# Optimization experiments

Measured on AMD Instinct MI355X. Metric: run time of the kernel, lower is better.

The kernel has to match this reference:

```python
import jax, jax.numpy as jnp
import numpy as np

NUM_LAYERS = 4
OPTIONS = 32
SHAPE = (3, 32, 32)
D = int(np.prod(SHAPE))  # 3072
H = 256
B = 256


def setup_inputs() -> dict:
    key = jax.random.key(0)
    ks = jax.random.split(key, 4)
    inputs = jax.random.normal(ks[0], (B,) + SHAPE, dtype=jnp.float32)
    Wb = jax.random.normal(ks[1], (D, H), dtype=jnp.float32) * 0.02
    bb = jnp.zeros((H,), dtype=jnp.float32)
    Wo_stack = jax.random.normal(ks[2], (NUM_LAYERS, H, OPTIONS * D), dtype=jnp.float32) * 0.02
    bo_stack = jnp.zeros((NUM_LAYERS, OPTIONS * D), dtype=jnp.float32)
    bias_stack = jnp.zeros((NUM_LAYERS, OPTIONS, D), dtype=jnp.float32)
    return {"inputs": inputs, "Wb": Wb, "bb": bb, "Wo_stack": Wo_stack,
            "bo_stack": bo_stack, "bias_stack": bias_stack}


def reference(inputs, Wb, bb, Wo_stack, bo_stack, bias_stack):
    """Iterative residual vector quantization (VQ-DRAW encoder).

    Returns (encodings [B, num_layers] int32, reconstructions [B, *SHAPE]).
    """
    b = inputs.shape[0]
    x = inputs.reshape(b, D)                      # [B, D] flattened target
    cur = jnp.zeros_like(x)                       # current reconstruction
    encodings = []
    for i in range(NUM_LAYERS):
        base_out = jax.nn.relu(cur @ Wb + bb)                     # [B, H]
        layer_out = (base_out @ Wo_stack[i] + bo_stack[i])        # [B, O*D]
        layer_out = layer_out.reshape(b, OPTIONS, D) + bias_stack[i][None]
        new = cur[:, None, :] + layer_out                          # [B, O, D]
        # per-(example, option) MSE-sum loss, fused argmin over options
        losses = jnp.sum(jnp.square(new - x[:, None, :]), axis=-1)  # [B, O]
        idx = jnp.argmin(losses, axis=-1)                          # [B]
        encodings.append(idx)
        cur = jnp.take_along_axis(new, idx[:, None, None], axis=1)[:, 0]  # [B, D]
    return jnp.stack(encodings, axis=-1), cur.reshape(inputs.shape)
```

## Files before the change

### kernel.cpp

```cpp
#include <hip/hip_runtime.h>
#include <hip/hip_bf16.h>

#define B_ 256
#define D_ 3072
#define H_ 256
#define OPT_ 32
#define OD_ 98304
#define NL_ 4

typedef __attribute__((ext_vector_type(8))) short short8;
typedef __attribute__((ext_vector_type(4))) float f32x4;

__device__ __forceinline__ unsigned short f2bf(float f) {
    unsigned int u = __float_as_uint(f);
    unsigned int r = (u + 0x7FFFu + ((u >> 16) & 1u)) >> 16;
    return (unsigned short)r;
}

__global__ __launch_bounds__(256) void init_kernel(const float* __restrict__ x,
                                                   float* __restrict__ cur,
                                                   float* __restrict__ rx,
                                                   float* __restrict__ zpart) {
    int gid0 = blockIdx.x * 256 + threadIdx.x;
    for (int g = gid0; g < B_ * D_; g += 131072) {
        cur[g] = 0.f;
        rx[g] = -x[g];
    }
    for (int g = gid0; g < 16 * B_ * H_; g += 131072) zpart[g] = 0.f;
}

__global__ __launch_bounds__(256) void gemm1_kernel(const float* __restrict__ cur,
                                                    const float* __restrict__ Wb,
                                                    float* __restrict__ zpart) {
    int t = threadIdx.x;
    int ks = blockIdx.x >> 5;
    int bg = blockIdx.x & 31;
    const float* wp = Wb + (size_t)ks * 192 * H_ + t;
    const float* cp = cur + (size_t)(bg * 8) * D_ + ks * 192;
    float acc[8] = {0.f, 0.f, 0.f, 0.f, 0.f, 0.f, 0.f, 0.f};
#pragma unroll 4
    for (int dd = 0; dd < 192; ++dd) {
        float w = wp[(size_t)dd * H_];
#pragma unroll
        for (int g = 0; g < 8; ++g) acc[g] += cp[(size_t)g * D_ + dd] * w;
    }
#pragma unroll
    for (int g = 0; g < 8; ++g)
        zpart[ks * (B_ * H_) + (bg * 8 + g) * H_ + t] = acc[g];
}

__global__ __launch_bounds__(256) void e_kernel(const float* __restrict__ zpart,
                                                const float* __restrict__ bb,
                                                unsigned char* __restrict__ base_ready,
                                                float* __restrict__ basef) {
    int m = blockIdx.x, k = threadIdx.x;
    float z = bb[k];
#pragma unroll
    for (int ks = 0; ks < 16; ++ks) z += zpart[ks * (B_ * H_) + m * H_ + k];
    z = z > 0.f ? z : 0.f;
    *(unsigned short*)(base_ready + (k >> 5) * 20480 + m * 80 + (k & 31) * 2) = f2bf(z);
    basef[m * H_ + k] = z;
}

__global__ __launch_bounds__(512, 4) void g2_kernel(const unsigned char* __restrict__ base_ready,
                                                    const float* __restrict__ Wo,
                                                    const float* __restrict__ biasL,
                                                    const float* __restrict__ boL,
                                                    const float* __restrict__ rx,
                                                    float* __restrict__ partial) {
    __shared__ __align__(16) unsigned char ldsA[2][20480];
    __shared__ __align__(16) unsigned char ldsW[2][10240];

    int t = threadIdx.x;
    int lane = t & 63, wv = t >> 6;
    int bx = blockIdx.x;
    int ncol0 = bx * 128;
    int o = bx / 24;
    int dbase = (bx % 24) * 128;

    int wm = wv >> 1, wn = wv & 1;
    int lrow = lane & 15, lk = lane >> 4;
    int nW = t & 127, kq = t >> 7;

    f32x4 acc[4][4];
#pragma unroll
    for (int mi = 0; mi < 4; ++mi)
#pragma unroll
        for (int ni = 0; ni < 4; ++ni) acc[mi][ni] = 0.f;

    float wfX[8], wfY[8];

#define DMA_A(S, BUF) {                                                                  \
    const unsigned char* gA = base_ready + (S) * 20480;                                  \
    __builtin_amdgcn_global_load_lds(                                                    \
        (const __attribute__((address_space(1))) unsigned int*)(gA + t * 16),            \
        (__attribute__((address_space(3))) unsigned int*)(&ldsA[BUF][0] + wv * 1024),    \
        16, 0, 0);                                                                       \
    __builtin_amdgcn_global_load_lds(                                                    \
        (const __attribute__((address_space(1))) unsigned int*)(gA + 8192 + t * 16),     \
        (__attribute__((address_space(3))) unsigned int*)(&ldsA[BUF][0] + 8192 + wv * 1024), \
        16, 0, 0);                                                                       \
    if (wv < 4)                                                                          \
        __builtin_amdgcn_global_load_lds(                                                \
            (const __attribute__((address_space(1))) unsigned int*)(gA + 16384 + t * 16),\
            (__attribute__((address_space(3))) unsigned int*)(&ldsA[BUF][0] + 16384 + wv * 1024), \
            16, 0, 0); }

#define LOADW_(S, WF) {                                                                  \
    const float* gp0 = Wo + (size_t)((S) * 32 + kq * 4) * OD_ + ncol0 + nW;              \
    WF[0] = gp0[0]; WF[1] = gp0[OD_]; WF[2] = gp0[2 * OD_]; WF[3] = gp0[3 * OD_];        \
    const float* gp1 = gp0 + (size_t)16 * OD_;                                           \
    WF[4] = gp1[0]; WF[5] = gp1[OD_]; WF[6] = gp1[2 * OD_]; WF[7] = gp1[3 * OD_]; }

#define WRITEW_(BUF, WF) {                                                               \
    uint2 pk0, pk1;                                                                      \
    pk0.x = (unsigned)f2bf(WF[0]) | ((unsigned)f2bf(WF[1]) << 16);                       \
    pk0.y = (unsigned)f2bf(WF[2]) | ((unsigned)f2bf(WF[3]) << 16);                       \
    *(uint2*)(ldsW[BUF] + nW * 80 + kq * 8) = pk0;                                       \
    pk1.x = (unsigned)f2bf(WF[4]) | ((unsigned)f2bf(WF[5]) << 16);                       \
    pk1.y = (unsigned)f2bf(WF[6]) | ((unsigned)f2bf(WF[7]) << 16);                       \
    *(uint2*)(ldsW[BUF] + nW * 80 + 32 + kq * 8) = pk1; }

    DMA_A(0, 0);
    LOADW_(0, wfX);
    LOADW_(1, wfY);
    WRITEW_(0, wfX);
    asm volatile("s_waitcnt lgkmcnt(0)" ::: "memory");
    __builtin_amdgcn_s_barrier();

#pragma unroll 2
    for (int s = 0; s < 8; ++s) {
        int cur = s & 1;
        if (s < 7) DMA_A(s + 1, cur ^ 1);
        if (s < 6) {
            if ((s & 1) == 0) { LOADW_(s + 2, wfX); }
            else              { LOADW_(s + 2, wfY); }
        }
        short8 bfr[4];
#pragma unroll
        for (int ni = 0; ni < 4; ++ni) {
            int nn = wn * 64 + ni * 16 + lrow;
            bfr[ni] = *(const short8*)(ldsW[cur] + nn * 80 + lk * 16);
        }
#pragma unroll
        for (int mi = 0; mi < 4; ++mi) {
            int row = wm * 64 + mi * 16 + lrow;
            short8 af = *(const short8*)(ldsA[cur] + row * 80 + lk * 16);
#pragma unroll
            for (int ni = 0; ni < 4; ++ni)
                acc[mi][ni] = __builtin_amdgcn_mfma_f32_16x16x32_bf16(af, bfr[ni], acc[mi][ni], 0, 0, 0);
        }
        if (s < 7) {
            if ((s & 1) == 0) { WRITEW_(cur ^ 1, wfY); }
            else              { WRITEW_(cur ^ 1, wfX); }
            if (s < 6) asm volatile("s_waitcnt vmcnt(8) lgkmcnt(0)" ::: "memory");
            else       asm volatile("s_waitcnt vmcnt(0) lgkmcnt(0)" ::: "memory");
            __builtin_amdgcn_s_barrier();
        }
    }

#undef DMA_A
#undef LOADW_
#undef WRITEW_

    float q[4];
#pragma unroll
    for (int ni = 0; ni < 4; ++ni) {
        int dcol = dbase + wn * 64 + ni * 16 + lrow;
        q[ni] = biasL[o * D_ + dcol] + boL[o * D_ + dcol];
    }
    float ssum[4][4];
#pragma unroll
    for (int mi = 0; mi < 4; ++mi)
#pragma unroll
        for (int r = 0; r < 4; ++r) ssum[mi][r] = 0.f;

#pragma unroll
    for (int mi = 0; mi < 4; ++mi) {
#pragma unroll
        for (int ni = 0; ni < 4; ++ni) {
            int dcol = dbase + wn * 64 + ni * 16 + lrow;
#pragma unroll
            for (int r = 0; r < 4; ++r) {
                int rowm = wm * 64 + mi * 16 + lk * 4 + r;
                float tv = acc[mi][ni][r] + rx[rowm * D_ + dcol] + q[ni];
                ssum[mi][r] += tv * tv;
            }
        }
    }
#pragma unroll
    for (int mi = 0; mi < 4; ++mi)
#pragma unroll
        for (int r = 0; r < 4; ++r) {
            float v = ssum[mi][r];
            v += __shfl_xor(v, 1);
            v += __shfl_xor(v, 2);
            v += __shfl_xor(v, 4);
            v += __shfl_xor(v, 8);
            if (lrow == 0) {
                int rowm = wm * 64 + mi * 16 + lk * 4 + r;
                partial[(rowm * OPT_ + o) * 48 + (bx % 24) * 2 + wn] = v;
            }
        }
}

__global__ __launch_bounds__(256) void c_kernel(const float* __restrict__ partial,
                                                int* __restrict__ idxbuf,
                                                float* __restrict__ enc, int layer) {
    __shared__ float ls[32];
    int b = blockIdx.x, t = threadIdx.x;
    int oo = t >> 3, j8 = t & 7;
    const float* pp = partial + (b * OPT_ + oo) * 48;
    float v = 0.f;
#pragma unroll
    for (int j = 0; j < 6; ++j) v += pp[j8 + 8 * j];
    v += __shfl_xor(v, 1);
    v += __shfl_xor(v, 2);
    v += __shfl_xor(v, 4);
    if (j8 == 0) ls[oo] = v;
    __syncthreads();
    if (t < 32) {
        float mv = ls[t];
        int mi = t;
#pragma unroll
        for (int m = 16; m >= 1; m >>= 1) {
            float ov = __shfl_xor(mv, m);
            int oi = __shfl_xor(mi, m);
            if (ov < mv || (ov == mv && oi < mi)) { mv = ov; mi = oi; }
        }
        if (t == 0) {
            idxbuf[b] = mi;
            enc[b * NL_ + layer] = (float)mi;
        }
    }
}

__global__ __launch_bounds__(256) void d_kernel(const int* __restrict__ idxbuf,
                                                const float* __restrict__ basef,
                                                const float* __restrict__ Wo,
                                                const float* __restrict__ boL,
                                                const float* __restrict__ biasL,
                                                const float* __restrict__ x,
                                                float* __restrict__ cur,
                                                float* __restrict__ rx) {
    __shared__ int sidx[256];
    __shared__ int scnt[32];
    __shared__ int snch[32];
    __shared__ int chunk_b[8];
    __shared__ float basL[8][256];
    int t = threadIdx.x;
    int dt = blockIdx.y;

    sidx[t] = idxbuf[t];
    __syncthreads();
    if (t < 32) {
        int c = 0;
        for (int b = 0; b < 256; ++b) c += (sidx[b] == t);
        scnt[t] = c;
        snch[t] = (c + 7) >> 3;
    }
    __syncthreads();
    int myo = sidx[t];
    int myrank = 0;
    for (int b = 0; b < t; ++b) myrank += (sidx[b] == myo);

    for (int j = blockIdx.x; ; j += 32) {
        int o = -1, ch = 0, pre = 0;
        for (int oo = 0; oo < 32; ++oo) {
            int n = snch[oo];
            if (j < pre + n) { o = oo; ch = j - pre; break; }
            pre += n;
        }
        if (o < 0) break;
        int cnt = scnt[o];
        int c0 = ch * 8;
        int rem = cnt - c0;
        if (rem > 8) rem = 8;

        __syncthreads();
        if (myo == o && myrank >= c0 && myrank < c0 + 8) chunk_b[myrank - c0] = t;
        __syncthreads();

        int bidx[8];
#pragma unroll
        for (int g = 0; g < 8; ++g) bidx[g] = chunk_b[(g < rem) ? g : (rem - 1)];
#pragma unroll
        for (int g = 0; g < 8; ++g) basL[g][t] = basef[bidx[g] * H_ + t];
        __syncthreads();

        int d = dt * 256 + t;
        const float* wp = Wo + (size_t)o * D_ + d;
        size_t nn = (size_t)o * D_ + d;
        float bov = boL[nn];
        float biv = biasL[nn];

        float acc[8] = {0.f, 0.f, 0.f, 0.f, 0.f, 0.f, 0.f, 0.f};
        for (int k0 = 0; k0 < 256; k0 += 8) {
            float w[8];
#pragma unroll
            for (int u = 0; u < 8; ++u) w[u] = wp[(size_t)(k0 + u) * OD_];
#pragma unroll
            for (int h = 0; h < 2; ++h) {
                int kb = k0 + h * 4;
                f32x4 bv[8];
#pragma unroll
                for (int g = 0; g < 8; ++g) bv[g] = *(const f32x4*)&basL[g][kb];
#pragma unroll
                for (int u = 0; u < 4; ++u) {
                    float wu = w[h * 4 + u];
#pragma unroll
                    for (int g = 0; g < 8; ++g) acc[g] += bv[g][u] * wu;
                }
            }
        }
#pragma unroll
        for (int g = 0; g < 8; ++g) {
            if (g < rem) {
                int b = bidx[g];
                float outv = cur[b * D_ + d] + acc[g] + bov + biv;
                cur[b * D_ + d] = outv;
                rx[b * D_ + d] = outv - x[b * D_ + d];
            }
        }
    }
}

extern "C" void kernel_launch(void* const* d_in, const int* in_sizes, int n_in,
                              void* d_out, int out_size, void* d_ws, size_t ws_size,
                              hipStream_t stream) {
    const float* x    = (const float*)d_in[0];
    const float* Wb   = (const float*)d_in[1];
    const float* bb   = (const float*)d_in[2];
    const float* Wo   = (const float*)d_in[3];
    const float* bo   = (const float*)d_in[4];
    const float* bias = (const float*)d_in[5];

    float* out = (float*)d_out;
    float* enc = out;
    float* cur = out + 1024;

    float* ws = (float*)d_ws;
    float* zpart   = ws;
    float* partial = ws + 1048576;
    float* rx      = ws + 1441792;
    float* basef   = ws + 2228224;
    unsigned char* base_ready = (unsigned char*)(ws + 2293760);
    int* idxbuf    = (int*)(ws + 2334720);

    init_kernel<<<512, 256, 0, stream>>>(x, cur, rx, zpart);

    for (int i = 0; i < NL_; ++i) {
        const float* WoL   = Wo + (size_t)i * H_ * OD_;
        const float* boLp  = bo + (size_t)i * OD_;
        const float* biasL = bias + (size_t)i * OD_;
        if (i > 0) gemm1_kernel<<<512, 256, 0, stream>>>(cur, Wb, zpart);
        e_kernel<<<256, 256, 0, stream>>>(zpart, bb, base_ready, basef);
        g2_kernel<<<768, 512, 0, stream>>>(base_ready, WoL, biasL, boLp, rx, partial);
        c_kernel<<<256, 256, 0, stream>>>(partial, idxbuf, enc, i);
        d_kernel<<<dim3(32, 12), 256, 0, stream>>>(idxbuf, basef, WoL, boLp, biasL, x, cur, rx);
    }
}
```

Measured before the change: 390.7 us.

## Make g2 a persistent atomic-ticket tile loop and shrink small-kernel grids

The output-projection GEMM kernel now launches 512 persistent blocks that take further tiles from a per-layer atomic ticket counter instead of one block per tile. This is meant to reduce tail imbalance and launch overhead across the 768 tiles. gemm1 uses half as many K-splits (each twice as long), which halves the zpart partial buffer and the reduction work in e_kernel. e_kernel and c_kernel each handle four rows per block with smaller grids. The trade-off is less parallelism in gemm1 and an extra atomic plus block syncs per tile in g2.

```diff
diff --git a/kernel.cpp b/kernel.cpp
--- a/kernel.cpp
+++ b/kernel.cpp
@@ -20,13 +20,15 @@
 __global__ __launch_bounds__(256) void init_kernel(const float* __restrict__ x,
                                                    float* __restrict__ cur,
                                                    float* __restrict__ rx,
-                                                   float* __restrict__ zpart) {
+                                                   float* __restrict__ zpart,
+                                                   int* __restrict__ g2tk) {
     int gid0 = blockIdx.x * 256 + threadIdx.x;
-    for (int g = gid0; g < B_ * D_; g += 131072) {
+    for (int g = gid0; g < B_ * D_; g += 65536) {
         cur[g] = 0.f;
         rx[g] = -x[g];
     }
-    for (int g = gid0; g < 16 * B_ * H_; g += 131072) zpart[g] = 0.f;
+    for (int g = gid0; g < 8 * B_ * H_; g += 65536) zpart[g] = 0.f;
+    if (gid0 < NL_) g2tk[gid0] = 512;
 }
 
 __global__ __launch_bounds__(256) void gemm1_kernel(const float* __restrict__ cur,
@@ -35,11 +37,11 @@
     int t = threadIdx.x;
     int ks = blockIdx.x >> 5;
     int bg = blockIdx.x & 31;
-    const float* wp = Wb + (size_t)ks * 192 * H_ + t;
-    const float* cp = cur + (size_t)(bg * 8) * D_ + ks * 192;
+    const float* wp = Wb + (size_t)ks * 384 * H_ + t;
+    const float* cp = cur + (size_t)(bg * 8) * D_ + ks * 384;
     float acc[8] = {0.f, 0.f, 0.f, 0.f, 0.f, 0.f, 0.f, 0.f};
 #pragma unroll 4
-    for (int dd = 0; dd < 192; ++dd) {
+    for (int dd = 0; dd < 384; ++dd) {
         float w = wp[(size_t)dd * H_];
 #pragma unroll
         for (int g = 0; g < 8; ++g) acc[g] += cp[(size_t)g * D_ + dd] * w;
@@ -53,13 +55,18 @@
                                                 const float* __restrict__ bb,
                                                 unsigned char* __restrict__ base_ready,
                                                 float* __restrict__ basef) {
-    int m = blockIdx.x, k = threadIdx.x;
-    float z = bb[k];
-#pragma unroll
-    for (int ks = 0; ks < 16; ++ks) z += zpart[ks * (B_ * H_) + m * H_ + k];
-    z = z > 0.f ? z : 0.f;
-    *(unsigned short*)(base_ready + (k >> 5) * 20480 + m * 80 + (k & 31) * 2) = f2bf(z);
-    basef[m * H_ + k] = z;
+    int k = threadIdx.x;
+    float bbk = bb[k];
+#pragma unroll
+    for (int mm = 0; mm < 4; ++mm) {
+        int m = blockIdx.x * 4 + mm;
+        float z = bbk;
+#pragma unroll
+        for (int ks = 0; ks < 8; ++ks) z += zpart[ks * (B_ * H_) + m * H_ + k];
+        z = z > 0.f ? z : 0.f;
+        *(unsigned short*)(base_ready + (k >> 5) * 20480 + m * 80 + (k & 31) * 2) = f2bf(z);
+        basef[m * H_ + k] = z;
+    }
 }
 
 __global__ __launch_bounds__(512, 4) void g2_kernel(const unsigned char* __restrict__ base_ready,
@@ -67,28 +74,17 @@
                                                     const float* __restrict__ biasL,
                                                     const float* __restrict__ boL,
                                                     const float* __restrict__ rx,
-                                                    float* __restrict__ partial) {
+                                                    float* __restrict__ partial,
+                                                    int* __restrict__ tk) {
     __shared__ __align__(16) unsigned char ldsA[2][20480];
     __shared__ __align__(16) unsigned char ldsW[2][10240];
+    __shared__ int s_next;
 
     int t = threadIdx.x;
     int lane = t & 63, wv = t >> 6;
-    int bx = blockIdx.x;
-    int ncol0 = bx * 128;
-    int o = bx / 24;
-    int dbase = (bx % 24) * 128;
-
     int wm = wv >> 1, wn = wv & 1;
     int lrow = lane & 15, lk = lane >> 4;
     int nW = t & 127, kq = t >> 7;
-
-    f32x4 acc[4][4];
-#pragma unroll
-    for (int mi = 0; mi < 4; ++mi)
-#pragma unroll
-        for (int ni = 0; ni < 4; ++ni) acc[mi][ni] = 0.f;
-
-    float wfX[8], wfY[8];
 
 #define DMA_A(S, BUF) {                                                                  \
     const unsigned char* gA = base_ready + (S) * 20480;                                  \
@@ -121,117 +117,139 @@
     pk1.y = (unsigned)f2bf(WF[6]) | ((unsigned)f2bf(WF[7]) << 16);                       \
     *(uint2*)(ldsW[BUF] + nW * 80 + 32 + kq * 8) = pk1; }
 
-    DMA_A(0, 0);
-    LOADW_(0, wfX);
-    LOADW_(1, wfY);
-    WRITEW_(0, wfX);
-    asm volatile("s_waitcnt lgkmcnt(0)" ::: "memory");
-    __builtin_amdgcn_s_barrier();
+    int tile = blockIdx.x;
+    while (tile < 768) {
+        int ncol0 = tile * 128;
+        int o = tile / 24;
+        int dbase = (tile % 24) * 128;
+
+        f32x4 acc[4][4];
+#pragma unroll
+        for (int mi = 0; mi < 4; ++mi)
+#pragma unroll
+            for (int ni = 0; ni < 4; ++ni) acc[mi][ni] = 0.f;
+
+        float wfX[8], wfY[8];
+
+        DMA_A(0, 0);
+        LOADW_(0, wfX);
+        LOADW_(1, wfY);
+        WRITEW_(0, wfX);
+        asm volatile("s_waitcnt lgkmcnt(0)" ::: "memory");
+        __builtin_amdgcn_s_barrier();
 
 #pragma unroll 2
-    for (int s = 0; s < 8; ++s) {
-        int cur = s & 1;
-        if (s < 7) DMA_A(s + 1, cur ^ 1);
-        if (s < 6) {
-            if ((s & 1) == 0) { LOADW_(s + 2, wfX); }
-            else              { LOADW_(s + 2, wfY); }
-        }
-        short8 bfr[4];
+        for (int s = 0; s < 8; ++s) {
+            int pb = s & 1;
+            if (s < 7) DMA_A(s + 1, pb ^ 1);
+            if (s < 6) {
+                if ((s & 1) == 0) { LOADW_(s + 2, wfX); }
+                else              { LOADW_(s + 2, wfY); }
+            }
+            short8 bfr[4];
+#pragma unroll
+            for (int ni = 0; ni < 4; ++ni) {
+                int nn = wn * 64 + ni * 16 + lrow;
+                bfr[ni] = *(const short8*)(ldsW[pb] + nn * 80 + lk * 16);
+            }
+#pragma unroll
+            for (int mi = 0; mi < 4; ++mi) {
+                int row = wm * 64 + mi * 16 + lrow;
+                short8 af = *(const short8*)(ldsA[pb] + row * 80 + lk * 16);
+#pragma unroll
+                for (int ni = 0; ni < 4; ++ni)
+                    acc[mi][ni] = __builtin_amdgcn_mfma_f32_16x16x32_bf16(af, bfr[ni], acc[mi][ni], 0, 0, 0);
+            }
+            if (s < 7) {
+                if ((s & 1) == 0) { WRITEW_(pb ^ 1, wfY); }
+                else              { WRITEW_(pb ^ 1, wfX); }
+                if (s < 6) asm volatile("s_waitcnt vmcnt(8) lgkmcnt(0)" ::: "memory");
+                else       asm volatile("s_waitcnt vmcnt(0) lgkmcnt(0)" ::: "memory");
+                __builtin_amdgcn_s_barrier();
+            }
+        }
+
+        float q[4];
 #pragma unroll
         for (int ni = 0; ni < 4; ++ni) {
-            int nn = wn * 64 + ni * 16 + lrow;
-            bfr[ni] = *(const short8*)(ldsW[cur] + nn * 80 + lk * 16);
-        }
+            int dcol = dbase + wn * 64 + ni * 16 + lrow;
+            q[ni] = biasL[o * D_ + dcol] + boL[o * D_ + dcol];
+        }
+        float ssum[4][4];
+#pragma unroll
+        for (int mi = 0; mi < 4; ++mi)
+#pragma unroll
+            for (int r = 0; r < 4; ++r) ssum[mi][r] = 0.f;
 #pragma unroll
         for (int mi = 0; mi < 4; ++mi) {
-            int row = wm * 64 + mi * 16 + lrow;
-            short8 af = *(const short8*)(ldsA[cur] + row * 80 + lk * 16);
-#pragma unroll
-            for (int ni = 0; ni < 4; ++ni)
-                acc[mi][ni] = __builtin_amdgcn_mfma_f32_16x16x32_bf16(af, bfr[ni], acc[mi][ni], 0, 0, 0);
-        }
-        if (s < 7) {
-            if ((s & 1) == 0) { WRITEW_(cur ^ 1, wfY); }
-            else              { WRITEW_(cur ^ 1, wfX); }
-            if (s < 6) asm volatile("s_waitcnt vmcnt(8) lgkmcnt(0)" ::: "memory");
-            else       asm volatile("s_waitcnt vmcnt(0) lgkmcnt(0)" ::: "memory");
-            __builtin_amdgcn_s_barrier();
-        }
-    }
-
+#pragma unroll
+            for (int ni = 0; ni < 4; ++ni) {
+                int dcol = dbase + wn * 64 + ni * 16 + lrow;
+#pragma unroll
+                for (int r = 0; r < 4; ++r) {
+                    int rowm = wm * 64 + mi * 16 + lk * 4 + r;
+                    float tv = acc[mi][ni][r] + rx[rowm * D_ + dcol] + q[ni];
+                    ssum[mi][r] += tv * tv;
+                }
+            }
+        }
+#pragma unroll
+        for (int mi = 0; mi < 4; ++mi)
+#pragma unroll
+            for (int r = 0; r < 4; ++r) {
+                float v = ssum[mi][r];
+                v += __shfl_xor(v, 1);
+                v += __shfl_xor(v, 2);
+                v += __shfl_xor(v, 4);
+                v += __shfl_xor(v, 8);
+                if (lrow == 0) {
+                    int rowm = wm * 64 + mi * 16 + lk * 4 + r;
+                    partial[(rowm * OPT_ + o) * 48 + (tile % 24) * 2 + wn] = v;
+                }
+            }
+
+        __syncthreads();
+        if (t == 0) s_next = atomicAdd(tk, 1);
+        __syncthreads();
+        tile = s_next;
+    }
 #undef DMA_A
 #undef LOADW_
 #undef WRITEW_
-
-    float q[4];
-#pragma unroll
-    for (int ni = 0; ni < 4; ++ni) {
-        int dcol = dbase + wn * 64 + ni * 16 + lrow;
-        q[ni] = biasL[o * D_ + dcol] + boL[o * D_ + dcol];
-    }
-    float ssum[4][4];
-#pragma unroll
-    for (int mi = 0; mi < 4; ++mi)
-#pragma unroll
-        for (int r = 0; r < 4; ++r) ssum[mi][r] = 0.f;
-
-#pragma unroll
-    for (int mi = 0; mi < 4; ++mi) {
-#pragma unroll
-        for (int ni = 0; ni < 4; ++ni) {
-            int dcol = dbase + wn * 64 + ni * 16 + lrow;
-#pragma unroll
-            for (int r = 0; r < 4; ++r) {
-                int rowm = wm * 64 + mi * 16 + lk * 4 + r;
-                float tv = acc[mi][ni][r] + rx[rowm * D_ + dcol] + q[ni];
-                ssum[mi][r] += tv * tv;
-            }
-        }
-    }
-#pragma unroll
-    for (int mi = 0; mi < 4; ++mi)
-#pragma unroll
-        for (int r = 0; r < 4; ++r) {
-            float v = ssum[mi][r];
-            v += __shfl_xor(v, 1);
-            v += __shfl_xor(v, 2);
-            v += __shfl_xor(v, 4);
-            v += __shfl_xor(v, 8);
-            if (lrow == 0) {
-                int rowm = wm * 64 + mi * 16 + lk * 4 + r;
-                partial[(rowm * OPT_ + o) * 48 + (bx % 24) * 2 + wn] = v;
-            }
-        }
 }
 
 __global__ __launch_bounds__(256) void c_kernel(const float* __restrict__ partial,
                                                 int* __restrict__ idxbuf,
                                                 float* __restrict__ enc, int layer) {
     __shared__ float ls[32];
-    int b = blockIdx.x, t = threadIdx.x;
+    int t = threadIdx.x;
     int oo = t >> 3, j8 = t & 7;
-    const float* pp = partial + (b * OPT_ + oo) * 48;
-    float v = 0.f;
-#pragma unroll
-    for (int j = 0; j < 6; ++j) v += pp[j8 + 8 * j];
-    v += __shfl_xor(v, 1);
-    v += __shfl_xor(v, 2);
-    v += __shfl_xor(v, 4);
-    if (j8 == 0) ls[oo] = v;
-    __syncthreads();
-    if (t < 32) {
-        float mv = ls[t];
-        int mi = t;
-#pragma unroll
-        for (int m = 16; m >= 1; m >>= 1) {
-            float ov = __shfl_xor(mv, m);
-            int oi = __shfl_xor(mi, m);
-            if (ov < mv || (ov == mv && oi < mi)) { mv = ov; mi = oi; }
-        }
-        if (t == 0) {
-            idxbuf[b] = mi;
-            enc[b * NL_ + layer] = (float)mi;
-        }
+    for (int bb2 = 0; bb2 < 4; ++bb2) {
+        int b = blockIdx.x * 4 + bb2;
+        const float* pp = partial + (b * OPT_ + oo) * 48;
+        float v = 0.f;
+#pragma unroll
+        for (int j = 0; j < 6; ++j) v += pp[j8 + 8 * j];
+        v += __shfl_xor(v, 1);
+        v += __shfl_xor(v, 2);
+        v += __shfl_xor(v, 4);
+        if (j8 == 0) ls[oo] = v;
+        __syncthreads();
+        if (t < 32) {
+            float mv = ls[t];
+            int mi = t;
+#pragma unroll
+            for (int m = 16; m >= 1; m >>= 1) {
+                float ov = __shfl_xor(mv, m);
+                int oi = __shfl_xor(mi, m);
+                if (ov < mv || (ov == mv && oi < mi)) { mv = ov; mi = oi; }
+            }
+            if (t == 0) {
+                idxbuf[b] = mi;
+                enc[b * NL_ + layer] = (float)mi;
+            }
+        }
+        __syncthreads();
     }
 }
 
@@ -341,22 +359,23 @@
 
     float* ws = (float*)d_ws;
     float* zpart   = ws;
-    float* partial = ws + 1048576;
-    float* rx      = ws + 1441792;
-    float* basef   = ws + 2228224;
-    unsigned char* base_ready = (unsigned char*)(ws + 2293760);
-    int* idxbuf    = (int*)(ws + 2334720);
-
-    init_kernel<<<512, 256, 0, stream>>>(x, cur, rx, zpart);
+    float* partial = ws + 524288;
+    float* rx      = ws + 917504;
+    float* basef   = ws + 1703936;
+    unsigned char* base_ready = (unsigned char*)(ws + 1769472);
+    int* idxbuf    = (int*)(ws + 1810432);
+    int* g2tk      = (int*)(ws + 1810688);
+
+    init_kernel<<<256, 256, 0, stream>>>(x, cur, rx, zpart, g2tk);
 
     for (int i = 0; i < NL_; ++i) {
         const float* WoL   = Wo + (size_t)i * H_ * OD_;
         const float* boLp  = bo + (size_t)i * OD_;
         const float* biasL = bias + (size_t)i * OD_;
-        if (i > 0) gemm1_kernel<<<512, 256, 0, stream>>>(cur, Wb, zpart);
-        e_kernel<<<256, 256, 0, stream>>>(zpart, bb, base_ready, basef);
-        g2_kernel<<<768, 512, 0, stream>>>(base_ready, WoL, biasL, boLp, rx, partial);
-        c_kernel<<<256, 256, 0, stream>>>(partial, idxbuf, enc, i);
+        if (i > 0) gemm1_kernel<<<256, 256, 0, stream>>>(cur, Wb, zpart);
+        e_kernel<<<64, 256, 0, stream>>>(zpart, bb, base_ready, basef);
+        g2_kernel<<<512, 512, 0, stream>>>(base_ready, WoL, biasL, boLp, rx, partial, g2tk + i);
+        c_kernel<<<64, 256, 0, stream>>>(partial, idxbuf, enc, i);
         d_kernel<<<dim3(32, 12), 256, 0, stream>>>(idxbuf, basef, WoL, boLp, biasL, x, cur, rx);
     }
 }
```

After: 500.4 us. 28.1% more time.

## Restructure g2 GEMM to 1024-thread blocks with A fragments loaded directly to registers

Applied to the files above, without the earlier changes.

The g2 kernel now uses 16 waves per block (4x4 wave grid), each computing a 64x32 sub-tile. The bf16 activation operand is loaded straight from global memory into registers instead of being staged into LDS with async DMA. Each stage now covers 64 K-rows split into two halves, which halves the number of barriers. The partial-sum layout widens from 48 to 96 entries per (row, option), so c_kernel and the workspace offsets change to match. The aim is more latency hiding and fewer barriers, at the cost of redundant global A reads across waves and more register pressure at 1024 threads.

```diff
diff --git a/kernel.cpp b/kernel.cpp
--- a/kernel.cpp
+++ b/kernel.cpp
@@ -62,111 +62,106 @@
     basef[m * H_ + k] = z;
 }
 
-__global__ __launch_bounds__(512, 4) void g2_kernel(const unsigned char* __restrict__ base_ready,
-                                                    const float* __restrict__ Wo,
-                                                    const float* __restrict__ biasL,
-                                                    const float* __restrict__ boL,
-                                                    const float* __restrict__ rx,
-                                                    float* __restrict__ partial) {
-    __shared__ __align__(16) unsigned char ldsA[2][20480];
-    __shared__ __align__(16) unsigned char ldsW[2][10240];
+__global__ __launch_bounds__(1024, 4) void g2_kernel(const unsigned char* __restrict__ base_ready,
+                                                     const float* __restrict__ Wo,
+                                                     const float* __restrict__ biasL,
+                                                     const float* __restrict__ boL,
+                                                     const float* __restrict__ rx,
+                                                     float* __restrict__ partial) {
+    __shared__ __align__(16) unsigned char ldsW[2][2][10240];
 
     int t = threadIdx.x;
     int lane = t & 63, wv = t >> 6;
-    int bx = blockIdx.x;
-    int ncol0 = bx * 128;
-    int o = bx / 24;
-    int dbase = (bx % 24) * 128;
-
-    int wm = wv >> 1, wn = wv & 1;
+    int tile = blockIdx.x;
+    int ncol0 = tile * 128;
+    int o = tile / 24;
+    int dbase = (tile % 24) * 128;
+
+    int wm = wv >> 2, wn = wv & 3;
     int lrow = lane & 15, lk = lane >> 4;
     int nW = t & 127, kq = t >> 7;
 
-    f32x4 acc[4][4];
+    f32x4 acc[4][2];
 #pragma unroll
     for (int mi = 0; mi < 4; ++mi)
 #pragma unroll
-        for (int ni = 0; ni < 4; ++ni) acc[mi][ni] = 0.f;
+        for (int ni = 0; ni < 2; ++ni) acc[mi][ni] = 0.f;
 
     float wfX[8], wfY[8];
-
-#define DMA_A(S, BUF) {                                                                  \
-    const unsigned char* gA = base_ready + (S) * 20480;                                  \
-    __builtin_amdgcn_global_load_lds(                                                    \
-        (const __attribute__((address_space(1))) unsigned int*)(gA + t * 16),            \
-        (__attribute__((address_space(3))) unsigned int*)(&ldsA[BUF][0] + wv * 1024),    \
-        16, 0, 0);                                                                       \
-    __builtin_amdgcn_global_load_lds(                                                    \
-        (const __attribute__((address_space(1))) unsigned int*)(gA + 8192 + t * 16),     \
-        (__attribute__((address_space(3))) unsigned int*)(&ldsA[BUF][0] + 8192 + wv * 1024), \
-        16, 0, 0);                                                                       \
-    if (wv < 4)                                                                          \
-        __builtin_amdgcn_global_load_lds(                                                \
-            (const __attribute__((address_space(1))) unsigned int*)(gA + 16384 + t * 16),\
-            (__attribute__((address_space(3))) unsigned int*)(&ldsA[BUF][0] + 16384 + wv * 1024), \
-            16, 0, 0); }
+    short8 afX[4], afY[4];
 
 #define LOADW_(S, WF) {                                                                  \
-    const float* gp0 = Wo + (size_t)((S) * 32 + kq * 4) * OD_ + ncol0 + nW;              \
-    WF[0] = gp0[0]; WF[1] = gp0[OD_]; WF[2] = gp0[2 * OD_]; WF[3] = gp0[3 * OD_];        \
-    const float* gp1 = gp0 + (size_t)16 * OD_;                                           \
-    WF[4] = gp1[0]; WF[5] = gp1[OD_]; WF[6] = gp1[2 * OD_]; WF[7] = gp1[3 * OD_]; }
+    const float* gp = Wo + (size_t)((S) * 64 + kq * 8) * OD_ + ncol0 + nW;               \
+    WF[0] = gp[0];            WF[1] = gp[OD_];                                           \
+    WF[2] = gp[2 * (size_t)OD_]; WF[3] = gp[3 * (size_t)OD_];                            \
+    WF[4] = gp[4 * (size_t)OD_]; WF[5] = gp[5 * (size_t)OD_];                            \
+    WF[6] = gp[6 * (size_t)OD_]; WF[7] = gp[7 * (size_t)OD_]; }
 
 #define WRITEW_(BUF, WF) {                                                               \
-    uint2 pk0, pk1;                                                                      \
-    pk0.x = (unsigned)f2bf(WF[0]) | ((unsigned)f2bf(WF[1]) << 16);                       \
-    pk0.y = (unsigned)f2bf(WF[2]) | ((unsigned)f2bf(WF[3]) << 16);                       \
-    *(uint2*)(ldsW[BUF] + nW * 80 + kq * 8) = pk0;                                       \
-    pk1.x = (unsigned)f2bf(WF[4]) | ((unsigned)f2bf(WF[5]) << 16);                       \
-    pk1.y = (unsigned)f2bf(WF[6]) | ((unsigned)f2bf(WF[7]) << 16);                       \
-    *(uint2*)(ldsW[BUF] + nW * 80 + 32 + kq * 8) = pk1; }
-
-    DMA_A(0, 0);
+    uint4 pk;                                                                            \
+    pk.x = (unsigned)f2bf(WF[0]) | ((unsigned)f2bf(WF[1]) << 16);                        \
+    pk.y = (unsigned)f2bf(WF[2]) | ((unsigned)f2bf(WF[3]) << 16);                        \
+    pk.z = (unsigned)f2bf(WF[4]) | ((unsigned)f2bf(WF[5]) << 16);                        \
+    pk.w = (unsigned)f2bf(WF[6]) | ((unsigned)f2bf(WF[7]) << 16);                        \
+    *(uint4*)(&ldsW[BUF][kq >> 2][0] + nW * 80 + (kq & 3) * 16) = pk; }
+
+#define AF_(G, AF) {                                                                     \
+    const unsigned char* gA = base_ready + (G) * 20480;                                  \
+    AF[0] = *(const short8*)(gA + (wm * 64 +  0 + lrow) * 80 + lk * 16);                 \
+    AF[1] = *(const short8*)(gA + (wm * 64 + 16 + lrow) * 80 + lk * 16);                 \
+    AF[2] = *(const short8*)(gA + (wm * 64 + 32 + lrow) * 80 + lk * 16);                 \
+    AF[3] = *(const short8*)(gA + (wm * 64 + 48 + lrow) * 80 + lk * 16); }
+
     LOADW_(0, wfX);
     LOADW_(1, wfY);
+    AF_(0, afX);
     WRITEW_(0, wfX);
     asm volatile("s_waitcnt lgkmcnt(0)" ::: "memory");
     __builtin_amdgcn_s_barrier();
 
 #pragma unroll 2
-    for (int s = 0; s < 8; ++s) {
+    for (int s = 0; s < 4; ++s) {
         int cur = s & 1;
-        if (s < 7) DMA_A(s + 1, cur ^ 1);
-        if (s < 6) {
+        AF_(2 * s + 1, afY);
+        if (s < 2) {
             if ((s & 1) == 0) { LOADW_(s + 2, wfX); }
             else              { LOADW_(s + 2, wfY); }
         }
-        short8 bfr[4];
-#pragma unroll
-        for (int ni = 0; ni < 4; ++ni) {
-            int nn = wn * 64 + ni * 16 + lrow;
-            bfr[ni] = *(const short8*)(ldsW[cur] + nn * 80 + lk * 16);
-        }
-#pragma unroll
-        for (int mi = 0; mi < 4; ++mi) {
-            int row = wm * 64 + mi * 16 + lrow;
-            short8 af = *(const short8*)(ldsA[cur] + row * 80 + lk * 16);
-#pragma unroll
-            for (int ni = 0; ni < 4; ++ni)
-                acc[mi][ni] = __builtin_amdgcn_mfma_f32_16x16x32_bf16(af, bfr[ni], acc[mi][ni], 0, 0, 0);
-        }
-        if (s < 7) {
+        short8 bfr0[2];
+#pragma unroll
+        for (int ni = 0; ni < 2; ++ni)
+            bfr0[ni] = *(const short8*)(&ldsW[cur][0][0] + (wn * 32 + ni * 16 + lrow) * 80 + lk * 16);
+#pragma unroll
+        for (int mi = 0; mi < 4; ++mi)
+#pragma unroll
+            for (int ni = 0; ni < 2; ++ni)
+                acc[mi][ni] = __builtin_amdgcn_mfma_f32_16x16x32_bf16(afX[mi], bfr0[ni], acc[mi][ni], 0, 0, 0);
+        if (s < 3) AF_(2 * s + 2, afX);
+        short8 bfr1[2];
+#pragma unroll
+        for (int ni = 0; ni < 2; ++ni)
+            bfr1[ni] = *(const short8*)(&ldsW[cur][1][0] + (wn * 32 + ni * 16 + lrow) * 80 + lk * 16);
+#pragma unroll
+        for (int mi = 0; mi < 4; ++mi)
+#pragma unroll
+            for (int ni = 0; ni < 2; ++ni)
+                acc[mi][ni] = __builtin_amdgcn_mfma_f32_16x16x32_bf16(afY[mi], bfr1[ni], acc[mi][ni], 0, 0, 0);
+        if (s < 3) {
             if ((s & 1) == 0) { WRITEW_(cur ^ 1, wfY); }
             else              { WRITEW_(cur ^ 1, wfX); }
-            if (s < 6) asm volatile("s_waitcnt vmcnt(8) lgkmcnt(0)" ::: "memory");
-            else       asm volatile("s_waitcnt vmcnt(0) lgkmcnt(0)" ::: "memory");
+            asm volatile("s_waitcnt lgkmcnt(0)" ::: "memory");
             __builtin_amdgcn_s_barrier();
         }
     }
 
-#undef DMA_A
 #undef LOADW_
 #undef WRITEW_
-
-    float q[4];
-#pragma unroll
-    for (int ni = 0; ni < 4; ++ni) {
-        int dcol = dbase + wn * 64 + ni * 16 + lrow;
+#undef AF_
+
+    float q[2];
+#pragma unroll
+    for (int ni = 0; ni < 2; ++ni) {
+        int dcol = dbase + wn * 32 + ni * 16 + lrow;
         q[ni] = biasL[o * D_ + dcol] + boL[o * D_ + dcol];
     }
     float ssum[4][4];
@@ -174,12 +169,11 @@
     for (int mi = 0; mi < 4; ++mi)
 #pragma unroll
         for (int r = 0; r < 4; ++r) ssum[mi][r] = 0.f;
-
 #pragma unroll
     for (int mi = 0; mi < 4; ++mi) {
 #pragma unroll
-        for (int ni = 0; ni < 4; ++ni) {
-            int dcol = dbase + wn * 64 + ni * 16 + lrow;
+        for (int ni = 0; ni < 2; ++ni) {
+            int dcol = dbase + wn * 32 + ni * 16 + lrow;
 #pragma unroll
             for (int r = 0; r < 4; ++r) {
                 int rowm = wm * 64 + mi * 16 + lk * 4 + r;
@@ -199,7 +193,7 @@
             v += __shfl_xor(v, 8);
             if (lrow == 0) {
                 int rowm = wm * 64 + mi * 16 + lk * 4 + r;
-                partial[(rowm * OPT_ + o) * 48 + (bx % 24) * 2 + wn] = v;
+                partial[(rowm * OPT_ + o) * 96 + (tile % 24) * 4 + wn] = v;
             }
         }
 }
@@ -210,10 +204,10 @@
     __shared__ float ls[32];
     int b = blockIdx.x, t = threadIdx.x;
     int oo = t >> 3, j8 = t & 7;
-    const float* pp = partial + (b * OPT_ + oo) * 48;
+    const float* pp = partial + (b * OPT_ + oo) * 96;
     float v = 0.f;
 #pragma unroll
-    for (int j = 0; j < 6; ++j) v += pp[j8 + 8 * j];
+    for (int j = 0; j < 12; ++j) v += pp[j8 + 8 * j];
     v += __shfl_xor(v, 1);
     v += __shfl_xor(v, 2);
     v += __shfl_xor(v, 4);
@@ -342,10 +336,10 @@
     float* ws = (float*)d_ws;
     float* zpart   = ws;
     float* partial = ws + 1048576;
-    float* rx      = ws + 1441792;
-    float* basef   = ws + 2228224;
-    unsigned char* base_ready = (unsigned char*)(ws + 2293760);
-    int* idxbuf    = (int*)(ws + 2334720);
+    float* rx      = ws + 1835008;
+    float* basef   = ws + 2621440;
+    unsigned char* base_ready = (unsigned char*)(ws + 2686976);
+    int* idxbuf    = (int*)(ws + 2727936);
 
     init_kernel<<<512, 256, 0, stream>>>(x, cur, rx, zpart);
 
@@ -355,7 +349,7 @@
         const float* biasL = bias + (size_t)i * OD_;
         if (i > 0) gemm1_kernel<<<512, 256, 0, stream>>>(cur, Wb, zpart);
         e_kernel<<<256, 256, 0, stream>>>(zpart, bb, base_ready, basef);
-        g2_kernel<<<768, 512, 0, stream>>>(base_ready, WoL, biasL, boLp, rx, partial);
+        g2_kernel<<<768, 1024, 0, stream>>>(base_ready, WoL, biasL, boLp, rx, partial);
         c_kernel<<<256, 256, 0, stream>>>(partial, idxbuf, enc, i);
         d_kernel<<<dim3(32, 12), 256, 0, stream>>>(idxbuf, basef, WoL, boLp, biasL, x, cur, rx);
     }
```

Result: slower. 452.4 us (+15.8%).

## Fuse next-layer base GEMM into gather kernel and drop init kernel

Applied to the files above, without the earlier changes.

Removes the separate init kernel by handling layer zero via flags (reading x with a negated sign, treating cur as zero) and removes the standalone gemm1 kernel. Each d_kernel block now multiplies its freshly computed reconstruction tile by the matching Wb slice and writes a per-dt partial, which e_kernel reduces over 12 partials instead of 16. This saves launches and rereading cur, but adds Wb reads inside d_kernel that are repeated per option group, plus extra block syncs.

```diff
diff --git a/kernel.cpp b/kernel.cpp
--- a/kernel.cpp
+++ b/kernel.cpp
@@ -17,46 +17,17 @@
     return (unsigned short)r;
 }
 
-__global__ __launch_bounds__(256) void init_kernel(const float* __restrict__ x,
-                                                   float* __restrict__ cur,
-                                                   float* __restrict__ rx,
-                                                   float* __restrict__ zpart) {
-    int gid0 = blockIdx.x * 256 + threadIdx.x;
-    for (int g = gid0; g < B_ * D_; g += 131072) {
-        cur[g] = 0.f;
-        rx[g] = -x[g];
-    }
-    for (int g = gid0; g < 16 * B_ * H_; g += 131072) zpart[g] = 0.f;
-}
-
-__global__ __launch_bounds__(256) void gemm1_kernel(const float* __restrict__ cur,
-                                                    const float* __restrict__ Wb,
-                                                    float* __restrict__ zpart) {
-    int t = threadIdx.x;
-    int ks = blockIdx.x >> 5;
-    int bg = blockIdx.x & 31;
-    const float* wp = Wb + (size_t)ks * 192 * H_ + t;
-    const float* cp = cur + (size_t)(bg * 8) * D_ + ks * 192;
-    float acc[8] = {0.f, 0.f, 0.f, 0.f, 0.f, 0.f, 0.f, 0.f};
-#pragma unroll 4
-    for (int dd = 0; dd < 192; ++dd) {
-        float w = wp[(size_t)dd * H_];
-#pragma unroll
-        for (int g = 0; g < 8; ++g) acc[g] += cp[(size_t)g * D_ + dd] * w;
-    }
-#pragma unroll
-    for (int g = 0; g < 8; ++g)
-        zpart[ks * (B_ * H_) + (bg * 8 + g) * H_ + t] = acc[g];
-}
-
-__global__ __launch_bounds__(256) void e_kernel(const float* __restrict__ zpart,
+__global__ __launch_bounds__(256) void e_kernel(const float* __restrict__ zpart2,
                                                 const float* __restrict__ bb,
                                                 unsigned char* __restrict__ base_ready,
-                                                float* __restrict__ basef) {
+                                                float* __restrict__ basef,
+                                                int first) {
     int m = blockIdx.x, k = threadIdx.x;
     float z = bb[k];
-#pragma unroll
-    for (int ks = 0; ks < 16; ++ks) z += zpart[ks * (B_ * H_) + m * H_ + k];
+    if (!first) {
+#pragma unroll
+        for (int dt = 0; dt < 12; ++dt) z += zpart2[dt * (B_ * H_) + m * H_ + k];
+    }
     z = z > 0.f ? z : 0.f;
     *(unsigned short*)(base_ready + (k >> 5) * 20480 + m * 80 + (k & 31) * 2) = f2bf(z);
     basef[m * H_ + k] = z;
@@ -66,7 +37,8 @@
                                                     const float* __restrict__ Wo,
                                                     const float* __restrict__ biasL,
                                                     const float* __restrict__ boL,
-                                                    const float* __restrict__ rx,
+                                                    const float* __restrict__ rp,
+                                                    float rsign,
                                                     float* __restrict__ partial) {
     __shared__ __align__(16) unsigned char ldsA[2][20480];
     __shared__ __align__(16) unsigned char ldsW[2][10240];
@@ -183,7 +155,7 @@
 #pragma unroll
             for (int r = 0; r < 4; ++r) {
                 int rowm = wm * 64 + mi * 16 + lk * 4 + r;
-                float tv = acc[mi][ni][r] + rx[rowm * D_ + dcol] + q[ni];
+                float tv = acc[mi][ni][r] + rsign * rp[rowm * D_ + dcol] + q[ni];
                 ssum[mi][r] += tv * tv;
             }
         }
@@ -241,8 +213,11 @@
                                                 const float* __restrict__ boL,
                                                 const float* __restrict__ biasL,
                                                 const float* __restrict__ x,
+                                                const float* __restrict__ Wb,
                                                 float* __restrict__ cur,
-                                                float* __restrict__ rx) {
+                                                float* __restrict__ rx,
+                                                float* __restrict__ zpart2,
+                                                int first, int last) {
     __shared__ int sidx[256];
     __shared__ int scnt[32];
     __shared__ int snch[32];
@@ -313,14 +288,36 @@
                 }
             }
         }
+        float fout[8] = {0.f, 0.f, 0.f, 0.f, 0.f, 0.f, 0.f, 0.f};
 #pragma unroll
         for (int g = 0; g < 8; ++g) {
             if (g < rem) {
                 int b = bidx[g];
-                float outv = cur[b * D_ + d] + acc[g] + bov + biv;
+                float cv = first ? 0.f : cur[b * D_ + d];
+                float outv = cv + acc[g] + bov + biv;
+                fout[g] = outv;
                 cur[b * D_ + d] = outv;
                 rx[b * D_ + d] = outv - x[b * D_ + d];
             }
+        }
+
+        if (!last) {
+            __syncthreads();
+#pragma unroll
+            for (int g = 0; g < 8; ++g) basL[g][t] = fout[g];
+            __syncthreads();
+            const float* wbp = Wb + (size_t)(dt * 256) * H_ + t;
+            float zacc[8] = {0.f, 0.f, 0.f, 0.f, 0.f, 0.f, 0.f, 0.f};
+#pragma unroll 4
+            for (int dd = 0; dd < 256; ++dd) {
+                float w = wbp[(size_t)dd * H_];
+#pragma unroll
+                for (int g = 0; g < 8; ++g) zacc[g] += basL[g][dd] * w;
+            }
+#pragma unroll
+            for (int g = 0; g < 8; ++g)
+                if (g < rem)
+                    zpart2[dt * (B_ * H_) + bidx[g] * H_ + t] = zacc[g];
         }
     }
 }
@@ -340,23 +337,23 @@
     float* cur = out + 1024;
 
     float* ws = (float*)d_ws;
-    float* zpart   = ws;
-    float* partial = ws + 1048576;
-    float* rx      = ws + 1441792;
-    float* basef   = ws + 2228224;
-    unsigned char* base_ready = (unsigned char*)(ws + 2293760);
-    int* idxbuf    = (int*)(ws + 2334720);
-
-    init_kernel<<<512, 256, 0, stream>>>(x, cur, rx, zpart);
+    float* zpart2  = ws;
+    float* partial = ws + 786432;
+    float* rx      = ws + 1179648;
+    float* basef   = ws + 1966080;
+    unsigned char* base_ready = (unsigned char*)(ws + 2031616);
+    int* idxbuf    = (int*)(ws + 2072576);
 
     for (int i = 0; i < NL_; ++i) {
         const float* WoL   = Wo + (size_t)i * H_ * OD_;
         const float* boLp  = bo + (size_t)i * OD_;
         const float* biasL = bias + (size_t)i * OD_;
-        if (i > 0) gemm1_kernel<<<512, 256, 0, stream>>>(cur, Wb, zpart);
-        e_kernel<<<256, 256, 0, stream>>>(zpart, bb, base_ready, basef);
-        g2_kernel<<<768, 512, 0, stream>>>(base_ready, WoL, biasL, boLp, rx, partial);
+        const float* rp    = (i == 0) ? x : rx;
+        float rsign        = (i == 0) ? -1.f : 1.f;
+        e_kernel<<<256, 256, 0, stream>>>(zpart2, bb, base_ready, basef, i == 0);
+        g2_kernel<<<768, 512, 0, stream>>>(base_ready, WoL, biasL, boLp, rp, rsign, partial);
         c_kernel<<<256, 256, 0, stream>>>(partial, idxbuf, enc, i);
-        d_kernel<<<dim3(32, 12), 256, 0, stream>>>(idxbuf, basef, WoL, boLp, biasL, x, cur, rx);
-    }
-}
+        d_kernel<<<dim3(32, 12), 256, 0, stream>>>(idxbuf, basef, WoL, boLp, biasL, x, Wb,
+                                                   cur, rx, zpart2, i == 0, i == NL_ - 1);
+    }
+}
```

New measurement: 389.6 us (median of 3 runs). About the same (-0.3%).
